# Optimization experiments

Measured on AMD Instinct MI355X. Metric: run time of the kernel, lower is better.

The kernel has to match this reference:

```python
import jax, jax.numpy as jnp
import numpy as np

KS, STRIDE, PAD, GROUPS = 7, 1, 3, 8


def setup_inputs() -> dict:
    key = jax.random.key(0)
    ks = jax.random.split(key, 6)
    B, C, H, W = 4, 128, 64, 64
    O = 128
    rel_size = O // GROUPS // 2  # 8
    return {
        "x": jax.random.normal(ks[0], (B, C, H, W), jnp.float32),
        "wq": jax.random.normal(ks[1], (O, C), jnp.float32) * 0.05,
        "wk": jax.random.normal(ks[2], (O, C), jnp.float32) * 0.05,
        "wv": jax.random.normal(ks[3], (O, C), jnp.float32) * 0.05,
        "rel_x": jax.random.normal(ks[4], (rel_size, KS), jnp.float32),
        "rel_y": jax.random.normal(ks[5], (O // GROUPS - rel_size, KS), jnp.float32),
    }


def _patches(a, fH, fW):
    # a: [B, C, pH, pW] -> [B, C, fH, fW, KS, KS] (overlapping windows, like torch unfold)
    cols = []
    for ki in range(KS):
        rows = []
        for kj in range(KS):
            rows.append(a[:, :, ki:ki + (fH - 1) * STRIDE + 1:STRIDE,
                             kj:kj + (fW - 1) * STRIDE + 1:STRIDE])
        cols.append(jnp.stack(rows, axis=-1))  # last axis = l (W-kernel)
    return jnp.stack(cols, axis=-2)            # second-to-last = k (H-kernel)


def reference(x, wq, wk, wv, rel_x, rel_y):
    B, C, H, W = x.shape
    O = wq.shape[0]
    rel_size = rel_x.shape[0]
    xp = jnp.pad(x, ((0, 0), (0, 0), (PAD, PAD), (PAD, PAD)))
    pH, pW = H + 2 * PAD, W + 2 * PAD
    fH, fW = (pH - KS) // STRIDE + 1, (pW - KS) // STRIDE + 1
    # 1x1 convs
    q = jnp.einsum('oc,bchw->bohw', wq, xp)
    k = jnp.einsum('oc,bchw->bohw', wk, xp)
    v = jnp.einsum('oc,bchw->bohw', wv, xp)
    h0 = (KS - 1) // 2
    win_q = q[:, :, h0:pH - KS // 2:STRIDE, h0:pW - KS // 2:STRIDE]  # [B,O,fH,fW]
    win_q_b = win_q.reshape(B, GROUPS, O // GROUPS, fH, fW)
    qx = win_q_b[:, :, :rel_size]
    qy = win_q_b[:, :, rel_size:]
    bias_x = jnp.einsum('bgxhw,xk->bhwk', qx, rel_x)  # varies along l (W-kernel)
    bias_y = jnp.einsum('bgyhw,yk->bhwk', qy, rel_y)  # varies along k (H-kernel)
    win_k = _patches(k, fH, fW)  # [B,O,fH,fW,KS,KS]
    win_v = _patches(v, fH, fW)
    logits = jnp.einsum('bchw,bchwkl->bhwkl', win_q, win_k)
    logits = logits + bias_x[:, :, :, None, :] + bias_y[:, :, :, :, None]
    attn = jax.nn.softmax(logits.reshape(B, fH, fW, KS * KS), axis=-1)
    attn = attn.reshape(B, fH, fW, KS, KS)
    out = jnp.einsum('bhwkl,bchwkl->bchw', attn, win_v)  # [B,O,fH,fW]
    return out
```

## Files before the change

kernel.cpp:

```cpp
#include <hip/hip_runtime.h>

typedef __fp16 half8_t __attribute__((ext_vector_type(8)));
typedef __fp16 h2_t    __attribute__((ext_vector_type(2)));
typedef float  f4_t    __attribute__((ext_vector_type(4)));

__device__ __forceinline__ h2_t u2h(unsigned u) { return __builtin_bit_cast(h2_t, u); }
__device__ __forceinline__ float dot2(unsigned k, unsigned q, float c) {
#if __has_builtin(__builtin_amdgcn_fdot2)
    return __builtin_amdgcn_fdot2(u2h(k), u2h(q), c, false);
#else
    h2_t kh = u2h(k), qh = u2h(q);
    return c + (float)kh[0] * (float)qh[0] + (float)kh[1] * (float)qh[1];
#endif
}
__device__ __forceinline__ unsigned pk(float a, float b) {
    return __builtin_bit_cast(unsigned, __builtin_amdgcn_cvt_pkrtz(a, b));
}

__global__ __launch_bounds__(256) void qkv_fused(
    const float* __restrict__ x, const float* __restrict__ wq,
    const float* __restrict__ wk, const float* __restrict__ wv,
    unsigned* __restrict__ qf, unsigned* __restrict__ kf,
    unsigned* __restrict__ vf)
{
    __shared__ __fp16 Af[2048 * 8];
    __shared__ float  tl4[4][16 * 17];

    const int tid = threadIdx.x, wvn = tid >> 6, lane = tid & 63;
    const int mtx = blockIdx.x >> 8;
    const int tg  = blockIdx.x & 255;
    const float* wsrc = (mtx == 0) ? wq : (mtx == 1 ? wk : wv);
    unsigned*    dst  = (mtx == 0) ? qf : (mtx == 1 ? kf : vf);

#pragma unroll
    for (int s = 0; s < 8; ++s) {
        const int it = s * 256 + tid;
        const int l = it & 63, ck = (it >> 6) & 3, ot = it >> 8;
        const float* wr = wsrc + (size_t)(ot * 16 + (l & 15)) * 128 + ck * 32 + (l >> 4) * 8;
        const float4 w0 = *(const float4*)wr;
        const float4 w1 = *(const float4*)(wr + 4);
        half8_t h;
        h[0] = (__fp16)w0.x; h[1] = (__fp16)w0.y; h[2] = (__fp16)w0.z; h[3] = (__fp16)w0.w;
        h[4] = (__fp16)w1.x; h[5] = (__fp16)w1.y; h[6] = (__fp16)w1.z; h[7] = (__fp16)w1.w;
        *(half8_t*)&Af[it * 8] = h;
    }

    const int t = tg * 4 + wvn;
    const int m = lane & 15, quad = lane >> 4;
    const int p0 = t * 16, b = p0 >> 12, hw = p0 & 4095;
    const float* xb = x + (size_t)b * (128 * 4096) + hw + m;
    half8_t B[4];
#pragma unroll
    for (int ck = 0; ck < 4; ++ck) {
        half8_t h;
#pragma unroll
        for (int j = 0; j < 8; ++j)
            h[j] = (__fp16)xb[(size_t)(ck * 32 + quad * 8 + j) * 4096];
        B[ck] = h;
    }
    __syncthreads();

    float* tl = tl4[wvn];
#pragma unroll
    for (int og = 0; og < 4; ++og) {
#pragma unroll
        for (int ot = 0; ot < 2; ++ot) {
            const int otile = og * 2 + ot;
            f4_t acc = {0.f, 0.f, 0.f, 0.f};
#pragma unroll
            for (int ck = 0; ck < 4; ++ck) {
                const half8_t A = *(const half8_t*)&Af[((otile * 4 + ck) * 64 + lane) * 8];
                acc = __builtin_amdgcn_mfma_f32_16x16x32_f16(A, B[ck], acc, 0, 0, 0);
            }
            const int c2l = ot * 8 + quad * 2;
            tl[m * 17 + c2l]     = __builtin_bit_cast(float, pk(acc[0], acc[1]));
            tl[m * 17 + c2l + 1] = __builtin_bit_cast(float, pk(acc[2], acc[3]));
        }
        __asm__ volatile("s_waitcnt lgkmcnt(0)" ::: "memory");
        __builtin_amdgcn_wave_barrier();
#pragma unroll
        for (int s = 0; s < 4; ++s) {
            const int px = s * 4 + quad;
            dst[(size_t)(p0 + px) * 64 + og * 16 + m] =
                __builtin_bit_cast(unsigned, tl[px * 17 + m]);
        }
        __builtin_amdgcn_wave_barrier();
    }
}

__global__ __launch_bounds__(1024) void attn_kernel(
    const unsigned* __restrict__ qf, const unsigned* __restrict__ kf,
    const unsigned* __restrict__ vf, const float* __restrict__ relx,
    const float* __restrict__ rely, float* __restrict__ out)
{
    __shared__ unsigned smem[19472];
    unsigned* kS    = smem;
    unsigned* vS    = smem + 9152;
    float*    rels  = (float*)(smem + 18304);
    float*    sxyL  = (float*)(smem + 18416);
    float*    biasL = (float*)(smem + 18960);
    float*    otile = (float*)smem;

    const int tid = threadIdx.x, bx = blockIdx.x;
    const int wv = tid >> 6, lane = tid & 63;
    const int w0 = (bx & 7) * 8;
    const int h0 = ((bx >> 3) & 15) * 4;
    const int b  = bx >> 7;
    const int dr = wv >> 2, dw0 = (wv & 3) * 2;

    if (tid < 112) rels[tid] = (tid < 56) ? relx[tid] : rely[tid - 56];

    for (int i = tid; i < 8960; i += 1024) {
        const int isv = i >= 4480;
        const int ii  = i - isv * 4480;
        const int pos = ii >> 5, c2 = (ii & 31) * 2;
        const int ri = pos / 14, ci = pos - ri * 14;
        const int r = h0 - 3 + ri, cw = w0 - 3 + ci;
        uint2 d = make_uint2(0u, 0u);
        if ((unsigned)r < 64u && (unsigned)cw < 64u) {
            const unsigned* src = isv ? vf : kf;
            d = *(const uint2*)(src + (size_t)((b * 4096 + r * 64 + cw) * 64 + c2));
        }
        unsigned* dstS = isv ? vS : kS;
        dstS[c2 * 143 + pos]       = d.x;
        dstS[(c2 + 1) * 143 + pos] = d.y;
    }

    if (tid < 512) {
        const int px = tid >> 4, tt = tid & 15;
        const int pix = b * 4096 + (h0 + (px >> 3)) * 64 + w0 + (px & 7);
        float s = 0.f;
#pragma unroll
        for (int g = 0; g < 8; ++g) {
            const h2_t hh = u2h(qf[(size_t)pix * 64 + g * 8 + (tt >> 1)]);
            s += (float)hh[tt & 1];
        }
        sxyL[px * 17 + tt] = s;
    }
    __syncthreads();

    if (tid < 448) {
        const int px = tid / 14, j = tid - px * 14;
        const int isy = j >= 7, jj = j - isy * 7;
        const float* sx = &sxyL[px * 17 + isy * 8];
        const float* rl = &rels[isy * 56 + jj];
        float s = 0.f;
#pragma unroll
        for (int i = 0; i < 8; ++i) s = fmaf(sx[i], rl[i * 7], s);
        biasL[px * 16 + j] = s;
    }
    __syncthreads();

    const int nn = (lane < 49) ? lane : 48;
    const int ki = (nn * 37) >> 8, kj = nn - ki * 7;
    const int pixu = __builtin_amdgcn_readfirstlane(
        b * 4096 + (h0 + dr) * 64 + (w0 + dw0));
    const uint4* qp0 = (const uint4*)(qf + (size_t)pixu * 64);
    const uint4* qp1 = (const uint4*)(qf + (size_t)(pixu + 1) * 64);
    const int pos = (dr + ki) * 14 + (dw0 + kj);
    float acc0 = 0.f, acc1 = 0.f;
#pragma unroll
    for (int c4 = 0; c4 < 16; ++c4) {
        const uint4 q0 = qp0[c4], q1 = qp1[c4];
        const unsigned* kb = &kS[(c4 * 4) * 143 + pos];
        unsigned lo, hi;
        lo = kb[0];       hi = kb[1];
        acc0 = dot2(lo, q0.x, acc0); acc1 = dot2(hi, q1.x, acc1);
        lo = kb[143];     hi = kb[144];
        acc0 = dot2(lo, q0.y, acc0); acc1 = dot2(hi, q1.y, acc1);
        lo = kb[286];     hi = kb[287];
        acc0 = dot2(lo, q0.z, acc0); acc1 = dot2(hi, q1.z, acc1);
        lo = kb[429];     hi = kb[430];
        acc0 = dot2(lo, q0.w, acc0); acc1 = dot2(hi, q1.w, acc1);
    }
    const int pxl0 = dr * 8 + dw0;
    int apk0, apk1;
    {
        const float* bb = &biasL[pxl0 * 16];
        float logit = (lane < 49) ? acc0 + bb[kj] + bb[7 + ki] : -1e30f;
        float mx = logit;
#pragma unroll
        for (int off = 32; off; off >>= 1) mx = fmaxf(mx, __shfl_xor(mx, off));
        const float e = __expf(logit - mx);
        float ss = e;
#pragma unroll
        for (int off = 32; off; off >>= 1) ss += __shfl_xor(ss, off);
        const float a = e / ss;
        apk0 = __builtin_bit_cast(int, __builtin_amdgcn_cvt_pkrtz(a, a));
    }
    {
        const float* bb = &biasL[(pxl0 + 1) * 16];
        float logit = (lane < 49) ? acc1 + bb[kj] + bb[7 + ki] : -1e30f;
        float mx = logit;
#pragma unroll
        for (int off = 32; off; off >>= 1) mx = fmaxf(mx, __shfl_xor(mx, off));
        const float e = __expf(logit - mx);
        float ss = e;
#pragma unroll
        for (int off = 32; off; off >>= 1) ss += __shfl_xor(ss, off);
        const float a = e / ss;
        apk1 = __builtin_bit_cast(int, __builtin_amdgcn_cvt_pkrtz(a, a));
    }
    __syncthreads();

    const int posb = dr * 14 + dw0;
    h2_t o0 = {(__fp16)0.f, (__fp16)0.f}, o1 = o0;
#pragma unroll
    for (int n = 0; n < 49; ++n) {
        const int nki = (n * 37) >> 8, nkj = n - nki * 7;
        const unsigned* vb = &vS[lane * 143 + posb + nki * 14 + nkj];
        const unsigned lo = vb[0], hi = vb[1];
        const h2_t a0 = u2h((unsigned)__builtin_amdgcn_readlane(apk0, n));
        const h2_t a1 = u2h((unsigned)__builtin_amdgcn_readlane(apk1, n));
        o0 += a0 * u2h(lo);
        o1 += a1 * u2h(hi);
    }
    *(float2*)&otile[(size_t)pxl0 * 130 + lane * 2] =
        make_float2((float)o0[0], (float)o0[1]);
    *(float2*)&otile[(size_t)(pxl0 + 1) * 130 + lane * 2] =
        make_float2((float)o1[0], (float)o1[1]);
    __syncthreads();

#pragma unroll
    for (int s = 0; s < 4; ++s) {
        const int i = s * 1024 + tid;
        const int pxl = i & 31, c = i >> 5;
        out[(size_t)(b * 128 + c) * 4096 + (h0 + (pxl >> 3)) * 64 + (w0 + (pxl & 7))] =
            otile[pxl * 130 + c];
    }
}

extern "C" void kernel_launch(void* const* d_in, const int* in_sizes, int n_in,
                              void* d_out, int out_size, void* d_ws, size_t ws_size,
                              hipStream_t stream) {
    const float* x    = (const float*)d_in[0];
    const float* wq   = (const float*)d_in[1];
    const float* wk   = (const float*)d_in[2];
    const float* wv   = (const float*)d_in[3];
    const float* relx = (const float*)d_in[4];
    const float* rely = (const float*)d_in[5];
    float* out = (float*)d_out;

    char* ws = (char*)d_ws;
    unsigned* qfb = (unsigned*)(ws);
    unsigned* kfb = (unsigned*)(ws + 0x400000);
    unsigned* vfb = (unsigned*)(ws + 0x800000);

    qkv_fused<<<dim3(768), 256, 0, stream>>>(x, wq, wk, wv, qfb, kfb, vfb);
    attn_kernel<<<dim3(512), 1024, 0, stream>>>(qfb, kfb, vfb, relx, rely, out);
}
```

Baseline: 103.3 us.

## Rewrite attention with MFMA for QK and AV, move bias into QKV kernel

```diff
diff --git a/kernel.cpp b/kernel.cpp
--- a/kernel.cpp
+++ b/kernel.cpp
@@ -1,18 +1,8 @@
 #include <hip/hip_runtime.h>
 
 typedef __fp16 half8_t __attribute__((ext_vector_type(8)));
-typedef __fp16 h2_t    __attribute__((ext_vector_type(2)));
 typedef float  f4_t    __attribute__((ext_vector_type(4)));
 
-__device__ __forceinline__ h2_t u2h(unsigned u) { return __builtin_bit_cast(h2_t, u); }
-__device__ __forceinline__ float dot2(unsigned k, unsigned q, float c) {
-#if __has_builtin(__builtin_amdgcn_fdot2)
-    return __builtin_amdgcn_fdot2(u2h(k), u2h(q), c, false);
-#else
-    h2_t kh = u2h(k), qh = u2h(q);
-    return c + (float)kh[0] * (float)qh[0] + (float)kh[1] * (float)qh[1];
-#endif
-}
 __device__ __forceinline__ unsigned pk(float a, float b) {
     return __builtin_bit_cast(unsigned, __builtin_amdgcn_cvt_pkrtz(a, b));
 }
@@ -20,17 +10,23 @@
 __global__ __launch_bounds__(256) void qkv_fused(
     const float* __restrict__ x, const float* __restrict__ wq,
     const float* __restrict__ wk, const float* __restrict__ wv,
+    const float* __restrict__ relx, const float* __restrict__ rely,
     unsigned* __restrict__ qf, unsigned* __restrict__ kf,
-    unsigned* __restrict__ vf)
+    unsigned* __restrict__ vf, float* __restrict__ biasG)
 {
     __shared__ __fp16 Af[2048 * 8];
     __shared__ float  tl4[4][16 * 17];
+    __shared__ float  sS[4][16 * 20];
+    __shared__ float  relsQ[120];
 
     const int tid = threadIdx.x, wvn = tid >> 6, lane = tid & 63;
     const int mtx = blockIdx.x >> 8;
     const int tg  = blockIdx.x & 255;
     const float* wsrc = (mtx == 0) ? wq : (mtx == 1 ? wk : wv);
     unsigned*    dst  = (mtx == 0) ? qf : (mtx == 1 ? kf : vf);
+
+    if (tid < 120)
+        relsQ[tid] = (tid < 56) ? relx[tid] : (tid < 112 ? rely[tid - 56] : 0.f);
 
 #pragma unroll
     for (int s = 0; s < 8; ++s) {
@@ -39,10 +35,9 @@
         const float* wr = wsrc + (size_t)(ot * 16 + (l & 15)) * 128 + ck * 32 + (l >> 4) * 8;
         const float4 w0 = *(const float4*)wr;
         const float4 w1 = *(const float4*)(wr + 4);
-        half8_t h;
-        h[0] = (__fp16)w0.x; h[1] = (__fp16)w0.y; h[2] = (__fp16)w0.z; h[3] = (__fp16)w0.w;
-        h[4] = (__fp16)w1.x; h[5] = (__fp16)w1.y; h[6] = (__fp16)w1.z; h[7] = (__fp16)w1.w;
-        *(half8_t*)&Af[it * 8] = h;
+        unsigned* d = (unsigned*)&Af[it * 8];
+        d[0] = pk(w0.x, w0.y); d[1] = pk(w0.z, w0.w);
+        d[2] = pk(w1.x, w1.y); d[3] = pk(w1.z, w1.w);
     }
 
     const int t = tg * 4 + wvn;
@@ -52,15 +47,17 @@
     half8_t B[4];
 #pragma unroll
     for (int ck = 0; ck < 4; ++ck) {
-        half8_t h;
-#pragma unroll
-        for (int j = 0; j < 8; ++j)
-            h[j] = (__fp16)xb[(size_t)(ck * 32 + quad * 8 + j) * 4096];
-        B[ck] = h;
+        float f[8];
+#pragma unroll
+        for (int j = 0; j < 8; ++j) f[j] = xb[(size_t)(ck * 32 + quad * 8 + j) * 4096];
+        unsigned* d = (unsigned*)&B[ck];
+        d[0] = pk(f[0], f[1]); d[1] = pk(f[2], f[3]);
+        d[2] = pk(f[4], f[5]); d[3] = pk(f[6], f[7]);
     }
     __syncthreads();
 
     float* tl = tl4[wvn];
+    float s0 = 0.f, s1 = 0.f, s2 = 0.f, s3 = 0.f;
 #pragma unroll
     for (int og = 0; og < 4; ++og) {
 #pragma unroll
@@ -72,6 +69,7 @@
                 const half8_t A = *(const half8_t*)&Af[((otile * 4 + ck) * 64 + lane) * 8];
                 acc = __builtin_amdgcn_mfma_f32_16x16x32_f16(A, B[ck], acc, 0, 0, 0);
             }
+            if (mtx == 0) { s0 += acc[0]; s1 += acc[1]; s2 += acc[2]; s3 += acc[3]; }
             const int c2l = ot * 8 + quad * 2;
             tl[m * 17 + c2l]     = __builtin_bit_cast(float, pk(acc[0], acc[1]));
             tl[m * 17 + c2l + 1] = __builtin_bit_cast(float, pk(acc[2], acc[3]));
@@ -86,147 +84,183 @@
         }
         __builtin_amdgcn_wave_barrier();
     }
-}
-
-__global__ __launch_bounds__(1024) void attn_kernel(
+
+    if (mtx == 0) {
+        f4_t sv = {s0, s1, s2, s3};
+        *(f4_t*)&sS[wvn][m * 20 + quad * 4] = sv;
+        __asm__ volatile("s_waitcnt lgkmcnt(0)" ::: "memory");
+        __builtin_amdgcn_wave_barrier();
+        f4_t bj = {0.f, 0.f, 0.f, 0.f};
+#pragma unroll
+        for (int jj = 0; jj < 4; ++jj) {
+            const int j = quad * 4 + jj;
+            float s = 0.f;
+            if (j < 7) {
+#pragma unroll
+                for (int tt = 0; tt < 8; ++tt)
+                    s = fmaf(sS[wvn][m * 20 + tt], relsQ[tt * 7 + j], s);
+            } else if (j < 14) {
+#pragma unroll
+                for (int tt = 0; tt < 8; ++tt)
+                    s = fmaf(sS[wvn][m * 20 + 8 + tt], relsQ[56 + tt * 7 + (j - 7)], s);
+            }
+            bj[jj] = s;
+        }
+        *(f4_t*)(biasG + (size_t)(p0 + m) * 16 + quad * 4) = bj;
+    }
+}
+
+__global__ __launch_bounds__(256) void attn_mfma(
     const unsigned* __restrict__ qf, const unsigned* __restrict__ kf,
-    const unsigned* __restrict__ vf, const float* __restrict__ relx,
-    const float* __restrict__ rely, float* __restrict__ out)
+    const unsigned* __restrict__ vf, const float* __restrict__ biasG,
+    float* __restrict__ out)
 {
-    __shared__ unsigned smem[19472];
-    unsigned* kS    = smem;
-    unsigned* vS    = smem + 9152;
-    float*    rels  = (float*)(smem + 18304);
-    float*    sxyL  = (float*)(smem + 18416);
-    float*    biasL = (float*)(smem + 18960);
-    float*    otile = (float*)smem;
+    __shared__ __fp16 vH[128 * 216];
+    __shared__ __fp16 aW[4 * 16 * 136];
+    __shared__ float  biasL[64 * 17];
 
     const int tid = threadIdx.x, bx = blockIdx.x;
     const int wv = tid >> 6, lane = tid & 63;
-    const int w0 = (bx & 7) * 8;
-    const int h0 = ((bx >> 3) & 15) * 4;
-    const int b  = bx >> 7;
-    const int dr = wv >> 2, dw0 = (wv & 3) * 2;
-
-    if (tid < 112) rels[tid] = (tid < 56) ? relx[tid] : rely[tid - 56];
-
-    for (int i = tid; i < 8960; i += 1024) {
-        const int isv = i >= 4480;
-        const int ii  = i - isv * 4480;
-        const int pos = ii >> 5, c2 = (ii & 31) * 2;
-        const int ri = pos / 14, ci = pos - ri * 14;
-        const int r = h0 - 3 + ri, cw = w0 - 3 + ci;
-        uint2 d = make_uint2(0u, 0u);
-        if ((unsigned)r < 64u && (unsigned)cw < 64u) {
-            const unsigned* src = isv ? vf : kf;
-            d = *(const uint2*)(src + (size_t)((b * 4096 + r * 64 + cw) * 64 + c2));
-        }
-        unsigned* dstS = isv ? vS : kS;
-        dstS[c2 * 143 + pos]       = d.x;
-        dstS[(c2 + 1) * 143 + pos] = d.y;
-    }
-
-    if (tid < 512) {
-        const int px = tid >> 4, tt = tid & 15;
+    const int n = lane & 15, quad = lane >> 4;
+    const int w0 = (bx & 7) * 8, h0 = ((bx >> 3) & 7) * 8, b = bx >> 6;
+
+    for (int i = tid; i < 1568; i += 256) {
+        const int pq = i >> 5, c2p = i & 31;
+        const int pos0 = pq * 4;
+        unsigned dx[4], dy[4];
+#pragma unroll
+        for (int p = 0; p < 4; ++p) {
+            const int pos = pos0 + p;
+            const int ri = (pos * 2341) >> 15;
+            const int ci = pos - ri * 14;
+            const int py = h0 - 3 + ri, px = w0 - 3 + ci;
+            uint2 d = make_uint2(0u, 0u);
+            if ((unsigned)py < 64u && (unsigned)px < 64u)
+                d = *(const uint2*)(vf + (size_t)((b * 4096 + py * 64 + px) * 64 + c2p * 2));
+            dx[p] = d.x; dy[p] = d.y;
+        }
+        const int c0 = c2p * 4;
+        *(uint2*)(vH + (c0 + 0) * 216 + pos0) = make_uint2(
+            __builtin_amdgcn_perm(dx[1], dx[0], 0x05040100u),
+            __builtin_amdgcn_perm(dx[3], dx[2], 0x05040100u));
+        *(uint2*)(vH + (c0 + 1) * 216 + pos0) = make_uint2(
+            __builtin_amdgcn_perm(dx[1], dx[0], 0x07060302u),
+            __builtin_amdgcn_perm(dx[3], dx[2], 0x07060302u));
+        *(uint2*)(vH + (c0 + 2) * 216 + pos0) = make_uint2(
+            __builtin_amdgcn_perm(dy[1], dy[0], 0x05040100u),
+            __builtin_amdgcn_perm(dy[3], dy[2], 0x05040100u));
+        *(uint2*)(vH + (c0 + 3) * 216 + pos0) = make_uint2(
+            __builtin_amdgcn_perm(dy[1], dy[0], 0x07060302u),
+            __builtin_amdgcn_perm(dy[3], dy[2], 0x07060302u));
+    }
+    for (int i = tid; i < 640; i += 256) {
+        const int c = i / 5, s = i - c * 5;
+        *(uint2*)(vH + c * 216 + 196 + s * 4) = make_uint2(0u, 0u);
+    }
+    for (int i = tid; i < 1024; i += 256) {
+        const int px = i >> 4, tt = i & 15;
         const int pix = b * 4096 + (h0 + (px >> 3)) * 64 + w0 + (px & 7);
-        float s = 0.f;
-#pragma unroll
-        for (int g = 0; g < 8; ++g) {
-            const h2_t hh = u2h(qf[(size_t)pix * 64 + g * 8 + (tt >> 1)]);
-            s += (float)hh[tt & 1];
-        }
-        sxyL[px * 17 + tt] = s;
+        biasL[px * 17 + tt] = biasG[(size_t)pix * 16 + tt];
     }
     __syncthreads();
 
-    if (tid < 448) {
-        const int px = tid / 14, j = tid - px * 14;
-        const int isy = j >= 7, jj = j - isy * 7;
-        const float* sx = &sxyL[px * 17 + isy * 8];
-        const float* rl = &rels[isy * 56 + jj];
-        float s = 0.f;
-#pragma unroll
-        for (int i = 0; i < 8; ++i) s = fmaf(sx[i], rl[i * 7], s);
-        biasL[px * 16 + j] = s;
-    }
-    __syncthreads();
-
-    const int nn = (lane < 49) ? lane : 48;
-    const int ki = (nn * 37) >> 8, kj = nn - ki * 7;
-    const int pixu = __builtin_amdgcn_readfirstlane(
-        b * 4096 + (h0 + dr) * 64 + (w0 + dw0));
-    const uint4* qp0 = (const uint4*)(qf + (size_t)pixu * 64);
-    const uint4* qp1 = (const uint4*)(qf + (size_t)(pixu + 1) * 64);
-    const int pos = (dr + ki) * 14 + (dw0 + kj);
-    float acc0 = 0.f, acc1 = 0.f;
-#pragma unroll
-    for (int c4 = 0; c4 < 16; ++c4) {
-        const uint4 q0 = qp0[c4], q1 = qp1[c4];
-        const unsigned* kb = &kS[(c4 * 4) * 143 + pos];
-        unsigned lo, hi;
-        lo = kb[0];       hi = kb[1];
-        acc0 = dot2(lo, q0.x, acc0); acc1 = dot2(hi, q1.x, acc1);
-        lo = kb[143];     hi = kb[144];
-        acc0 = dot2(lo, q0.y, acc0); acc1 = dot2(hi, q1.y, acc1);
-        lo = kb[286];     hi = kb[287];
-        acc0 = dot2(lo, q0.z, acc0); acc1 = dot2(hi, q1.z, acc1);
-        lo = kb[429];     hi = kb[430];
-        acc0 = dot2(lo, q0.w, acc0); acc1 = dot2(hi, q1.w, acc1);
-    }
-    const int pxl0 = dr * 8 + dw0;
-    int apk0, apk1;
+    const int wrow = h0 + wv * 2;
+    uint4 qA[4];
+#pragma unroll
+    for (int kc = 0; kc < 4; ++kc) {
+        const int pix = b * 4096 + (wrow + (n >> 3)) * 64 + w0 + (n & 7);
+        qA[kc] = *(const uint4*)(qf + (size_t)pix * 64 + kc * 16 + quad * 4);
+    }
+    f4_t lg[7];
+#pragma unroll
+    for (int t = 0; t < 7; ++t) {
+        const int posL = t * 16 + n;
+        const int ri = (posL * 2341) >> 15;
+        const int ci = posL - ri * 14;
+        const int py = wrow - 3 + ri, pxc = w0 - 3 + ci;
+        const bool val = ((unsigned)py < 64u) && ((unsigned)pxc < 64u);
+        const int pix = b * 4096 + py * 64 + pxc;
+        f4_t acc = {0.f, 0.f, 0.f, 0.f};
+#pragma unroll
+        for (int kc = 0; kc < 4; ++kc) {
+            uint4 kB = make_uint4(0u, 0u, 0u, 0u);
+            if (val) kB = *(const uint4*)(kf + (size_t)pix * 64 + kc * 16 + quad * 4);
+            acc = __builtin_amdgcn_mfma_f32_16x16x32_f16(
+                __builtin_bit_cast(half8_t, qA[kc]),
+                __builtin_bit_cast(half8_t, kB), acc, 0, 0, 0);
+        }
+        lg[t] = acc;
+    }
+
+    const int pad = (wv & 1) * 4;
     {
-        const float* bb = &biasL[pxl0 * 16];
-        float logit = (lane < 49) ? acc0 + bb[kj] + bb[7 + ki] : -1e30f;
-        float mx = logit;
-#pragma unroll
-        for (int off = 32; off; off >>= 1) mx = fmaxf(mx, __shfl_xor(mx, off));
-        const float e = __expf(logit - mx);
-        float ss = e;
-#pragma unroll
-        for (int off = 32; off; off >>= 1) ss += __shfl_xor(ss, off);
-        const float a = e / ss;
-        apk0 = __builtin_bit_cast(int, __builtin_amdgcn_cvt_pkrtz(a, a));
-    }
-    {
-        const float* bb = &biasL[(pxl0 + 1) * 16];
-        float logit = (lane < 49) ? acc1 + bb[kj] + bb[7 + ki] : -1e30f;
-        float mx = logit;
-#pragma unroll
-        for (int off = 32; off; off >>= 1) mx = fmaxf(mx, __shfl_xor(mx, off));
-        const float e = __expf(logit - mx);
-        float ss = e;
-#pragma unroll
-        for (int off = 32; off; off >>= 1) ss += __shfl_xor(ss, off);
-        const float a = e / ss;
-        apk1 = __builtin_bit_cast(int, __builtin_amdgcn_cvt_pkrtz(a, a));
-    }
-    __syncthreads();
-
-    const int posb = dr * 14 + dw0;
-    h2_t o0 = {(__fp16)0.f, (__fp16)0.f}, o1 = o0;
-#pragma unroll
-    for (int n = 0; n < 49; ++n) {
-        const int nki = (n * 37) >> 8, nkj = n - nki * 7;
-        const unsigned* vb = &vS[lane * 143 + posb + nki * 14 + nkj];
-        const unsigned lo = vb[0], hi = vb[1];
-        const h2_t a0 = u2h((unsigned)__builtin_amdgcn_readlane(apk0, n));
-        const h2_t a1 = u2h((unsigned)__builtin_amdgcn_readlane(apk1, n));
-        o0 += a0 * u2h(lo);
-        o1 += a1 * u2h(hi);
-    }
-    *(float2*)&otile[(size_t)pxl0 * 130 + lane * 2] =
-        make_float2((float)o0[0], (float)o0[1]);
-    *(float2*)&otile[(size_t)(pxl0 + 1) * 130 + lane * 2] =
-        make_float2((float)o1[0], (float)o1[1]);
-    __syncthreads();
-
-#pragma unroll
-    for (int s = 0; s < 4; ++s) {
-        const int i = s * 1024 + tid;
-        const int pxl = i & 31, c = i >> 5;
-        out[(size_t)(b * 128 + c) * 4096 + (h0 + (pxl >> 3)) * 64 + (w0 + (pxl & 7))] =
-            otile[pxl * 130 + c];
+        const int row = lane >> 2, ch = lane & 3;
+        const int off = pad ? (ch == 0 ? 0 : 112 + pad + (ch - 1) * 4)
+                            : 112 + ch * 4;
+        *(uint2*)(aW + wv * 2176 + row * 136 + off) = make_uint2(0u, 0u);
+    }
+#pragma unroll
+    for (int i = 0; i < 4; ++i) {
+        const int px = quad * 4 + i;
+        const int dr = px >> 3, dw = px & 7;
+        const float* bb = &biasL[(wv * 16 + px) * 17];
+        float mx = -1e30f;
+#pragma unroll
+        for (int t = 0; t < 7; ++t) {
+            const int posL = t * 16 + n;
+            const int ri = (posL * 2341) >> 15;
+            const int ci = posL - ri * 14;
+            const unsigned ki = ri - dr, kj = ci - dw;
+            float v = -1e30f;
+            if (ki < 7u && kj < 7u) v = lg[t][i] + bb[kj] + bb[7 + ki];
+            lg[t][i] = v;
+            mx = fmaxf(mx, v);
+        }
+        mx = fmaxf(mx, __shfl_xor(mx, 1));
+        mx = fmaxf(mx, __shfl_xor(mx, 2));
+        mx = fmaxf(mx, __shfl_xor(mx, 4));
+        mx = fmaxf(mx, __shfl_xor(mx, 8));
+        float ss = 0.f;
+#pragma unroll
+        for (int t = 0; t < 7; ++t) {
+            const float e = __expf(lg[t][i] - mx);
+            lg[t][i] = e;
+            ss += e;
+        }
+        ss += __shfl_xor(ss, 1);
+        ss += __shfl_xor(ss, 2);
+        ss += __shfl_xor(ss, 4);
+        ss += __shfl_xor(ss, 8);
+        const float inv = 1.f / ss;
+#pragma unroll
+        for (int t = 0; t < 7; ++t)
+            aW[wv * 2176 + px * 136 + pad + t * 16 + n] = (__fp16)(lg[t][i] * inv);
+    }
+    __asm__ volatile("s_waitcnt lgkmcnt(0)" ::: "memory");
+    __builtin_amdgcn_wave_barrier();
+
+    const int startw = wv * 28 - pad;
+    uint4 pA[4];
+#pragma unroll
+    for (int kc = 0; kc < 4; ++kc)
+        pA[kc] = *(const uint4*)(aW + wv * 2176 + n * 136 + kc * 32 + quad * 8);
+#pragma unroll
+    for (int tn = 0; tn < 8; ++tn) {
+        f4_t acc = {0.f, 0.f, 0.f, 0.f};
+#pragma unroll
+        for (int kc = 0; kc < 4; ++kc) {
+            const half8_t vB = *(const half8_t*)(vH + (tn * 16 + n) * 216 +
+                                                 startw + kc * 32 + quad * 8);
+            acc = __builtin_amdgcn_mfma_f32_16x16x32_f16(
+                __builtin_bit_cast(half8_t, pA[kc]), vB, acc, 0, 0, 0);
+        }
+        const int c = tn * 16 + n;
+#pragma unroll
+        for (int i = 0; i < 4; ++i) {
+            const int px = quad * 4 + i;
+            const int hwp = (wrow + (px >> 3)) * 64 + w0 + (px & 7);
+            out[(size_t)(b * 128 + c) * 4096 + hwp] = acc[i];
+        }
     }
 }
 
@@ -245,7 +279,9 @@
     unsigned* qfb = (unsigned*)(ws);
     unsigned* kfb = (unsigned*)(ws + 0x400000);
     unsigned* vfb = (unsigned*)(ws + 0x800000);
-
-    qkv_fused<<<dim3(768), 256, 0, stream>>>(x, wq, wk, wv, qfb, kfb, vfb);
-    attn_kernel<<<dim3(512), 1024, 0, stream>>>(qfb, kfb, vfb, relx, rely, out);
-}
+    float*    bG  = (float*)   (ws + 0xC00000);
+
+    qkv_fused<<<dim3(768), 256, 0, stream>>>(x, wq, wk, wv, relx, rely,
+                                             qfb, kfb, vfb, bG);
+    attn_mfma<<<dim3(256), 256, 0, stream>>>(qfb, kfb, vfb, bG, out);
+}
```

Result: faster. 97.41 us (-5.7%).
